# Kernel tuning notes

Measured on AMD Instinct MI355X. Metric: run time of the kernel, lower is better.

The kernel has to match this reference:

```python
import jax, jax.numpy as jnp
import numpy as np

EPS = 1e-5

def _batchnorm1d(x, gamma, beta):
    # x: [B, C, L]; BatchNorm1d(C) training-mode stats over (B, L) per channel
    m = x.mean(axis=(0, 2), keepdims=True)
    v = ((x - m) ** 2).mean(axis=(0, 2), keepdims=True)  # biased variance
    return (x - m) / jnp.sqrt(v + EPS) * gamma[None, :, None] + beta[None, :, None]

def setup_inputs() -> dict:
    key = jax.random.key(0)
    ks = jax.random.split(key, 12)
    B, N, K, D = 1024, 50, 8, 128
    NUM_ENTS, NUM_RELS = 500000, 1000
    inp = {
        'hrt': jax.random.randint(ks[0], (B, 3), 0, NUM_RELS, dtype=jnp.int64) if jax.config.read('jax_enable_x64') else jax.random.randint(ks[0], (B, 3), 0, NUM_RELS).astype(jnp.int32),
        'neb': jax.random.randint(ks[1], (B, N), 0, NUM_ENTS).astype(jnp.int32),
        'nebr': jax.random.randint(ks[2], (B, N, K), 0, NUM_RELS).astype(jnp.int32),
        'adj': jax.random.uniform(ks[3], (B, N + 1, N + 1), dtype=jnp.float32),
        'ent_W': jax.random.normal(ks[4], (NUM_ENTS, D), dtype=jnp.float32) * 0.02,
        'rel_W': jax.random.normal(ks[5], (NUM_RELS, D), dtype=jnp.float32) * 0.02,
        'att_W': jax.random.normal(ks[6], (D, D), dtype=jnp.float32) * (1.0 / np.sqrt(D)),
        'att_b': jnp.zeros((D,), dtype=jnp.float32),
        'gcn_W': jax.random.normal(ks[7], (D, D), dtype=jnp.float32) * (1.0 / np.sqrt(D)),
        'gcn_b': jnp.zeros((D,), dtype=jnp.float32),
        'bn_gamma': jnp.ones((N + 1,), dtype=jnp.float32),
        'bn_beta': jnp.zeros((N + 1,), dtype=jnp.float32),
    }
    return inp

def reference(hrt, neb, nebr, adj, ent_W, rel_W, att_W, att_b, gcn_W, gcn_b, bn_gamma, bn_beta):
    h_em = ent_W[hrt[:, 0]][:, None, :]   # [B,1,D]
    t_em = ent_W[hrt[:, 2]][:, None, :]
    r_em = rel_W[hrt[:, 1]][:, None, :]
    neb_e = ent_W[neb]                    # [B,N,D]
    neb_r_mean = rel_W[nebr].mean(axis=2) # [B,N,D]  (mean over K neighbor relations)
    sum_hrt = (h_em + t_em + r_em) / 3.0  # mean over the 3 stacked rows -> [B,1,D]
    subg = (neb_e + neb_r_mean) / 2.0     # [B,N,D]
    # attention: att_fc applied to query and keys, then bmm
    q = sum_hrt @ att_W.T + att_b         # [B,1,D]
    kmat = subg @ att_W.T + att_b         # [B,N,D]
    att = jnp.einsum('bod,bnd->bn', q, kmat)  # [B,N]
    att = jax.nn.leaky_relu(att, 0.01)
    att = jax.nn.softmax(att, axis=-1)
    subg_w = att[:, :, None] * subg       # [B,N,D]
    x = jnp.concatenate([sum_hrt, subg_w], axis=1)  # [B,N+1,D]
    x = x @ gcn_W.T + gcn_b
    # GCN layer 1 (dropout is identity in eval)
    g1 = _batchnorm1d(jax.nn.relu(jnp.einsum('bij,bjd->bid', adj, x)), bn_gamma, bn_beta)
    # GCN layer 2
    g2 = _batchnorm1d(jax.nn.relu(jnp.einsum('bij,bjd->bid', adj, g1)), bn_gamma, bn_beta)
    tri_em = g2[:, 0:1, :]                # [B,1,D]
    return (h_em, t_em, r_em, tri_em)
```

## Files before the change

### kernel.cpp

```cpp
#include <hip/hip_runtime.h>

#define Bb 1024
#define NN 50
#define KK 8
#define DD 128
#define CC 51

typedef __attribute__((ext_vector_type(8))) short short8;
typedef __attribute__((ext_vector_type(4))) float f32x4;

__device__ __forceinline__ unsigned short f2bf(float f) {
  union { float f; unsigned int u; } un; un.f = f;
  unsigned int r = un.u + 0x7fffu + ((un.u >> 16) & 1u);
  return (unsigned short)(r >> 16);
}
__device__ __forceinline__ float bf2f(unsigned short h) {
  union { unsigned int u; float f; } un; un.u = ((unsigned int)h) << 16;
  return un.f;
}

static constexpr size_t SZ_BCD   = (size_t)Bb * CC * DD;
static constexpr size_t BYTES_H1 = SZ_BCD * 2;
static constexpr size_t OFF_BN   = BYTES_H1;
static constexpr size_t OFF_H2   = OFF_BN + 1024;

__global__ __launch_bounds__(256, 4) void kA_fused(
    const int* __restrict__ hrt, const int* __restrict__ neb,
    const int* __restrict__ nebr, const float* __restrict__ entW,
    const float* __restrict__ relW, const float* __restrict__ attW,
    const float* __restrict__ attb, const float* __restrict__ gcnW,
    const float* __restrict__ gcnb, const float* __restrict__ adj,
    unsigned short* __restrict__ H1bf, float* __restrict__ bn1,
    float* __restrict__ out) {
  int b = blockIdx.x, t = threadIdx.x;
  __shared__ __align__(16) float sub[52 * 132];
  __shared__ float Al[51 * 52];
  __shared__ float sq[DD], sw[DD];
  __shared__ float sl[NN];
  __shared__ float cval;
  unsigned short* Xbl = (unsigned short*)sub;

  for (int idx = t; idx < 51 * 52; idx += 256) {
    int i = idx / 52, j = idx - i * 52;
    Al[idx] = (j < 51) ? adj[(size_t)b * (CC * CC) + i * CC + j] : 0.f;
  }
  if (t < 32) {
    int hi = hrt[b * 3 + 0], ri = hrt[b * 3 + 1], ti = hrt[b * 3 + 2];
    float4 hv = ((const float4*)(entW + (size_t)hi * DD))[t];
    float4 tv = ((const float4*)(entW + (size_t)ti * DD))[t];
    float4 rv = ((const float4*)(relW + (size_t)ri * DD))[t];
    ((float4*)(out + (size_t)b * DD))[t] = hv;
    ((float4*)(out + (size_t)Bb * DD + (size_t)b * DD))[t] = tv;
    ((float4*)(out + (size_t)2 * Bb * DD + (size_t)b * DD))[t] = rv;
    const float inv3 = 1.f / 3.f;
    float4 s;
    s.x = (hv.x + tv.x + rv.x) * inv3;
    s.y = (hv.y + tv.y + rv.y) * inv3;
    s.z = (hv.z + tv.z + rv.z) * inv3;
    s.w = (hv.w + tv.w + rv.w) * inv3;
    ((float4*)sub)[t] = s;
    ((float4*)(sub + 51 * 132))[t] = make_float4(0.f, 0.f, 0.f, 0.f);
  }
  for (int idx = t; idx < NN * 32; idx += 256) {
    int r = idx >> 5, c4 = idx & 31;
    int e = neb[b * NN + r];
    float4 ev = ((const float4*)(entW + (size_t)e * DD))[c4];
    const int* rb = nebr + ((size_t)(b * NN + r)) * KK;
    float4 rs = make_float4(0.f, 0.f, 0.f, 0.f);
#pragma unroll
    for (int k = 0; k < KK; ++k) {
      float4 rv = ((const float4*)(relW + (size_t)rb[k] * DD))[c4];
      rs.x += rv.x; rs.y += rv.y; rs.z += rv.z; rs.w += rv.w;
    }
    float4 sg;
    sg.x = 0.5f * (ev.x + rs.x * 0.125f);
    sg.y = 0.5f * (ev.y + rs.y * 0.125f);
    sg.z = 0.5f * (ev.z + rs.z * 0.125f);
    sg.w = 0.5f * (ev.w + rs.w * 0.125f);
    ((float4*)(sub + (r + 1) * 132))[c4] = sg;
  }
  __syncthreads();
  {
    int wv = t >> 6, l = t & 63, half = l >> 5, l32 = l & 31;
    float4 sv = ((const float4*)sub)[l32];
#pragma unroll 4
    for (int j = 0; j < 16; ++j) {
      int d = 32 * wv + 2 * j + half;
      float4 wr = ((const float4*)(attW + (size_t)d * DD))[l32];
      float p = wr.x * sv.x + wr.y * sv.y + wr.z * sv.z + wr.w * sv.w;
#pragma unroll
      for (int m = 1; m < 32; m <<= 1) p += __shfl_xor(p, m);
      if (l32 == 0) sq[d] = p + attb[d];
    }
  }
  __syncthreads();
  if (t < 128) {
    float w0 = 0.f, w1 = 0.f, w2 = 0.f, w3 = 0.f;
    const float* wc = attW + t;
#pragma unroll 8
    for (int k = 0; k < 128; k += 4) {
      w0 += sq[k]     * wc[(size_t)k * DD];
      w1 += sq[k + 1] * wc[(size_t)(k + 1) * DD];
      w2 += sq[k + 2] * wc[(size_t)(k + 2) * DD];
      w3 += sq[k + 3] * wc[(size_t)(k + 3) * DD];
    }
    sw[t] = (w0 + w1) + (w2 + w3);
  } else if (t < 192) {
    int l = t - 128;
    float v = sq[l] * attb[l] + sq[l + 64] * attb[l + 64];
#pragma unroll
    for (int m = 1; m < 64; m <<= 1) v += __shfl_xor(v, m);
    if (l == 0) cval = v;
  }
  __syncthreads();
  if (t < NN * 4) {
    int n = t >> 2, q = t & 3;
    const float* sg = sub + (n + 1) * 132 + q * 32;
    const float* wq = sw + q * 32;
    float L = 0.f;
#pragma unroll 8
    for (int e = 0; e < 32; ++e) L += sg[e] * wq[e];
    L += __shfl_xor(L, 1);
    L += __shfl_xor(L, 2);
    if (q == 0) {
      L += cval;
      sl[n] = (L > 0.f) ? L : 0.01f * L;
    }
  }
  __syncthreads();
  if (t < 64) {
    float v = (t < NN) ? sl[t] : -1e30f;
    float mx = v;
#pragma unroll
    for (int m = 1; m < 64; m <<= 1) mx = fmaxf(mx, __shfl_xor(mx, m));
    float e = (t < NN) ? __expf(v - mx) : 0.f;
    float sm = e;
#pragma unroll
    for (int m = 1; m < 64; m <<= 1) sm += __shfl_xor(sm, m);
    if (t < NN) sl[t] = e / sm;
  }
  __syncthreads();
  {
    int wv = t >> 6, lane = t & 63;
    int wm = wv >> 1, wn = wv & 1;
    int m16 = lane & 15, g = lane >> 4, q8 = g * 8;
    f32x4 acc[2][4] = {};
    int rowA[2]; float sc[2];
#pragma unroll
    for (int mt = 0; mt < 2; ++mt) {
      int row = wm * 32 + mt * 16 + m16;
      rowA[mt] = (row <= 51) ? row : 51;
      sc[mt] = (row == 0) ? 1.f : ((row <= 50) ? sl[row - 1] : 0.f);
    }
#pragma unroll
    for (int ks = 0; ks < 4; ++ks) {
      short8 afr[2];
#pragma unroll
      for (int mt = 0; mt < 2; ++mt) {
        const float* ap = sub + rowA[mt] * 132 + ks * 32 + q8;
        float4 v0 = ((const float4*)ap)[0];
        float4 v1 = ((const float4*)ap)[1];
        short8 a;
        a[0] = (short)f2bf(sc[mt] * v0.x); a[1] = (short)f2bf(sc[mt] * v0.y);
        a[2] = (short)f2bf(sc[mt] * v0.z); a[3] = (short)f2bf(sc[mt] * v0.w);
        a[4] = (short)f2bf(sc[mt] * v1.x); a[5] = (short)f2bf(sc[mt] * v1.y);
        a[6] = (short)f2bf(sc[mt] * v1.z); a[7] = (short)f2bf(sc[mt] * v1.w);
        afr[mt] = a;
      }
#pragma unroll
      for (int nt = 0; nt < 4; ++nt) {
        int n = wn * 64 + nt * 16 + m16;
        const float* bp = gcnW + (size_t)n * DD + ks * 32 + q8;
        float4 b0 = ((const float4*)bp)[0];
        float4 b1 = ((const float4*)bp)[1];
        short8 bf;
        bf[0] = (short)f2bf(b0.x); bf[1] = (short)f2bf(b0.y);
        bf[2] = (short)f2bf(b0.z); bf[3] = (short)f2bf(b0.w);
        bf[4] = (short)f2bf(b1.x); bf[5] = (short)f2bf(b1.y);
        bf[6] = (short)f2bf(b1.z); bf[7] = (short)f2bf(b1.w);
        acc[0][nt] = __builtin_amdgcn_mfma_f32_16x16x32_bf16(afr[0], bf, acc[0][nt], 0, 0, 0);
        acc[1][nt] = __builtin_amdgcn_mfma_f32_16x16x32_bf16(afr[1], bf, acc[1][nt], 0, 0, 0);
      }
    }
    __syncthreads();
    int qd = g * 4;
#pragma unroll
    for (int mt = 0; mt < 2; ++mt) {
#pragma unroll
      for (int nt = 0; nt < 4; ++nt) {
        int col = wn * 64 + nt * 16 + m16;
        float bias = gcnb[col];
#pragma unroll
        for (int r = 0; r < 4; ++r) {
          int row = wm * 32 + mt * 16 + qd + r;
          if (row < 52) Xbl[row * 136 + col] = f2bf(acc[mt][nt][r] + bias);
        }
      }
    }
  }
  __syncthreads();
  {
    int tc = t & 15, tr = t >> 4;
    float4 acc0[4], acc1[4];
#pragma unroll
    for (int k = 0; k < 4; ++k) {
      acc0[k] = make_float4(0.f, 0.f, 0.f, 0.f);
      acc1[k] = make_float4(0.f, 0.f, 0.f, 0.f);
    }
    for (int jj4 = 0; jj4 < 13; ++jj4) {
      float4 av[4];
#pragma unroll
      for (int k = 0; k < 4; ++k) {
        int i = tr + 16 * k;
        av[k] = (i < 51) ? ((const float4*)(Al + i * 52))[jj4]
                         : make_float4(0.f, 0.f, 0.f, 0.f);
      }
#pragma unroll
      for (int ee = 0; ee < 4; ++ee) {
        int jj = jj4 * 4 + ee;
        uint4 v = ((const uint4*)(Xbl + jj * 136))[tc];
        float f0 = bf2f((unsigned short)(v.x & 0xffff));
        float f1 = bf2f((unsigned short)(v.x >> 16));
        float f2 = bf2f((unsigned short)(v.y & 0xffff));
        float f3 = bf2f((unsigned short)(v.y >> 16));
        float f4 = bf2f((unsigned short)(v.z & 0xffff));
        float f5 = bf2f((unsigned short)(v.z >> 16));
        float f6 = bf2f((unsigned short)(v.w & 0xffff));
        float f7 = bf2f((unsigned short)(v.w >> 16));
#pragma unroll
        for (int k = 0; k < 4; ++k) {
          float a = (ee == 0) ? av[k].x : (ee == 1) ? av[k].y
                    : (ee == 2) ? av[k].z : av[k].w;
          acc0[k].x += a * f0; acc0[k].y += a * f1;
          acc0[k].z += a * f2; acc0[k].w += a * f3;
          acc1[k].x += a * f4; acc1[k].y += a * f5;
          acc1[k].z += a * f6; acc1[k].w += a * f7;
        }
      }
    }
#pragma unroll
    for (int k = 0; k < 4; ++k) {
      int i = tr + 16 * k;
      if (i < 51) {
        float4 h0, h1v;
        h0.x = fmaxf(acc0[k].x, 0.f); h0.y = fmaxf(acc0[k].y, 0.f);
        h0.z = fmaxf(acc0[k].z, 0.f); h0.w = fmaxf(acc0[k].w, 0.f);
        h1v.x = fmaxf(acc1[k].x, 0.f); h1v.y = fmaxf(acc1[k].y, 0.f);
        h1v.z = fmaxf(acc1[k].z, 0.f); h1v.w = fmaxf(acc1[k].w, 0.f);
        size_t rowoff = ((size_t)b * CC + i) * DD;
        ushort4 p0, p1;
        p0.x = f2bf(h0.x); p0.y = f2bf(h0.y); p0.z = f2bf(h0.z); p0.w = f2bf(h0.w);
        p1.x = f2bf(h1v.x); p1.y = f2bf(h1v.y); p1.z = f2bf(h1v.z); p1.w = f2bf(h1v.w);
        ((ushort4*)(H1bf + rowoff))[2 * tc]     = p0;
        ((ushort4*)(H1bf + rowoff))[2 * tc + 1] = p1;
        float s = h0.x + h0.y + h0.z + h0.w + h1v.x + h1v.y + h1v.z + h1v.w;
        float qq = h0.x * h0.x + h0.y * h0.y + h0.z * h0.z + h0.w * h0.w +
                   h1v.x * h1v.x + h1v.y * h1v.y + h1v.z * h1v.z + h1v.w * h1v.w;
#pragma unroll
        for (int m = 1; m < 16; m <<= 1) {
          s += __shfl_xor(s, m);
          qq += __shfl_xor(qq, m);
        }
        if (tc == 0) {
          atomicAdd(&bn1[i], s);
          atomicAdd(&bn1[64 + i], qq);
        }
      }
    }
  }
}

__global__ __launch_bounds__(128) void k6_row0(
    const unsigned short* __restrict__ H1bf, const float* __restrict__ adj,
    const float* __restrict__ bn1, const float* __restrict__ gamma,
    const float* __restrict__ beta, float* __restrict__ h2,
    float* __restrict__ bn2) {
  __shared__ float cj[52];
  __shared__ float td[64];
  __shared__ float reds[128], redq[128];
  int b = blockIdx.x, t = threadIdx.x;
  const float invBD = 1.f / ((float)Bb * (float)DD);
  if (t < 64) td[t] = 0.f;
  if (t < 51) {
    float s = bn1[t], q = bn1[64 + t];
    float m = s * invBD;
    float v = fmaxf(q * invBD - m * m, 0.f);
    float inv = rsqrtf(v + 1e-5f);
    float al = gamma[t] * inv;
    float de = beta[t] - m * al;
    float a0 = adj[(size_t)b * (CC * CC) + t];
    cj[t] = a0 * al;
    td[t] = a0 * de;
  }
  __syncthreads();
  float tcst = 0.f;
  for (int j = 0; j < 51; ++j) tcst += td[j];
  float acc = tcst;
  const unsigned short* hb = H1bf + (size_t)b * CC * DD + t;
#pragma unroll 4
  for (int j = 0; j < 51; ++j) acc += cj[j] * bf2f(hb[(size_t)j * DD]);
  acc = fmaxf(acc, 0.f);
  h2[(size_t)b * DD + t] = acc;
  reds[t] = acc;
  redq[t] = acc * acc;
  __syncthreads();
  for (int s = 64; s > 0; s >>= 1) {
    if (t < s) { reds[t] += reds[t + s]; redq[t] += redq[t + s]; }
    __syncthreads();
  }
  if (t == 0) {
    atomicAdd(&bn2[0], reds[0]);
    atomicAdd(&bn2[1], redq[0]);
  }
}

__global__ __launch_bounds__(256) void k8_final(
    const float* __restrict__ h2, const float* __restrict__ bn2,
    const float* __restrict__ gamma, const float* __restrict__ beta,
    float* __restrict__ out) {
  int i = blockIdx.x * 256 + threadIdx.x;
  const float invBD = 1.f / ((float)Bb * (float)DD);
  float m = bn2[0] * invBD;
  float v = fmaxf(bn2[1] * invBD - m * m, 0.f);
  float inv = rsqrtf(v + 1e-5f);
  out[(size_t)3 * Bb * DD + i] = (h2[i] - m) * inv * gamma[0] + beta[0];
}

extern "C" void kernel_launch(void* const* d_in, const int* in_sizes, int n_in,
                              void* d_out, int out_size, void* d_ws, size_t ws_size,
                              hipStream_t stream) {
  (void)in_sizes; (void)n_in; (void)out_size; (void)ws_size;
  const int*   hrt   = (const int*)d_in[0];
  const int*   neb   = (const int*)d_in[1];
  const int*   nebr  = (const int*)d_in[2];
  const float* adj   = (const float*)d_in[3];
  const float* entW  = (const float*)d_in[4];
  const float* relW  = (const float*)d_in[5];
  const float* attW  = (const float*)d_in[6];
  const float* attb  = (const float*)d_in[7];
  const float* gcnW  = (const float*)d_in[8];
  const float* gcnb  = (const float*)d_in[9];
  const float* gamma = (const float*)d_in[10];
  const float* beta  = (const float*)d_in[11];
  float* out = (float*)d_out;
  char*  ws  = (char*)d_ws;

  unsigned short* H1bf = (unsigned short*)ws;
  float*          bn1  = (float*)(ws + OFF_BN);
  float*          bn2  = bn1 + 128;
  float*          h2   = (float*)(ws + OFF_H2);

  hipMemsetAsync((void*)bn1, 0, 1024, stream);

  kA_fused<<<Bb, 256, 0, stream>>>(hrt, neb, nebr, entW, relW, attW, attb,
                                   gcnW, gcnb, adj, H1bf, bn1, out);
  k6_row0<<<Bb, 128, 0, stream>>>(H1bf, adj, bn1, gamma, beta, h2, bn2);
  k8_final<<<(Bb * DD) / 256, 256, 0, stream>>>(h2, bn2, gamma, beta, out);
}
```

Before: 481.4 us.

## Fuse all stages into one persistent kernel with grid barriers and LDS-resident H1

Merges the three kernels into a single kernel that uses two software grid barriers, one after each BatchNorm statistics accumulation. The bf16 H1 activations stay in shared memory instead of making a round trip through global memory, and the h2 buffer and final elementwise kernel are removed. The intent is to drop two launches and the H1 and h2 global traffic. The cost is that 1024 blocks must all be co-resident for the spin barriers; with launch bounds of 4 blocks per CU on 256 CUs this just fits, and if it does not the kernel deadlocks. Blocks also idle while they spin at each barrier.

After: 677.8 us. 40.8% more time.

```diff
diff --git a/kernel.cpp b/kernel.cpp
--- a/kernel.cpp
+++ b/kernel.cpp
@@ -19,19 +19,28 @@
   return un.f;
 }
 
-static constexpr size_t SZ_BCD   = (size_t)Bb * CC * DD;
-static constexpr size_t BYTES_H1 = SZ_BCD * 2;
-static constexpr size_t OFF_BN   = BYTES_H1;
-static constexpr size_t OFF_H2   = OFF_BN + 1024;
-
-__global__ __launch_bounds__(256, 4) void kA_fused(
+__device__ __forceinline__ void grid_barrier(unsigned* cnt) {
+  __syncthreads();
+  if (threadIdx.x == 0) {
+    __threadfence();
+    atomicAdd(cnt, 1u);
+    while (__hip_atomic_load(cnt, __ATOMIC_RELAXED, __HIP_MEMORY_SCOPE_AGENT) <
+           (unsigned)gridDim.x) {
+      __builtin_amdgcn_s_sleep(2);
+    }
+  }
+  __syncthreads();
+  __threadfence();
+}
+
+__global__ __launch_bounds__(256, 4) void kAll(
     const int* __restrict__ hrt, const int* __restrict__ neb,
     const int* __restrict__ nebr, const float* __restrict__ entW,
     const float* __restrict__ relW, const float* __restrict__ attW,
     const float* __restrict__ attb, const float* __restrict__ gcnW,
     const float* __restrict__ gcnb, const float* __restrict__ adj,
-    unsigned short* __restrict__ H1bf, float* __restrict__ bn1,
-    float* __restrict__ out) {
+    const float* __restrict__ gamma, const float* __restrict__ beta,
+    float* __restrict__ bnbuf, float* __restrict__ out) {
   int b = blockIdx.x, t = threadIdx.x;
   __shared__ __align__(16) float sub[52 * 132];
   __shared__ float Al[51 * 52];
@@ -39,6 +48,9 @@
   __shared__ float sl[NN];
   __shared__ float cval;
   unsigned short* Xbl = (unsigned short*)sub;
+  unsigned short* H1l = (unsigned short*)sub + 7072;
+  unsigned* cnt1 = (unsigned*)(bnbuf + 160);
+  unsigned* cnt2 = (unsigned*)(bnbuf + 161);
 
   for (int idx = t; idx < 51 * 52; idx += 256) {
     int i = idx / 52, j = idx - i * 52;
@@ -247,12 +259,12 @@
         h0.z = fmaxf(acc0[k].z, 0.f); h0.w = fmaxf(acc0[k].w, 0.f);
         h1v.x = fmaxf(acc1[k].x, 0.f); h1v.y = fmaxf(acc1[k].y, 0.f);
         h1v.z = fmaxf(acc1[k].z, 0.f); h1v.w = fmaxf(acc1[k].w, 0.f);
-        size_t rowoff = ((size_t)b * CC + i) * DD;
         ushort4 p0, p1;
         p0.x = f2bf(h0.x); p0.y = f2bf(h0.y); p0.z = f2bf(h0.z); p0.w = f2bf(h0.w);
         p1.x = f2bf(h1v.x); p1.y = f2bf(h1v.y); p1.z = f2bf(h1v.z); p1.w = f2bf(h1v.w);
-        ((ushort4*)(H1bf + rowoff))[2 * tc]     = p0;
-        ((ushort4*)(H1bf + rowoff))[2 * tc + 1] = p1;
+        ushort4* hrow = (ushort4*)(H1l + i * DD);
+        hrow[2 * tc]     = p0;
+        hrow[2 * tc + 1] = p1;
         float s = h0.x + h0.y + h0.z + h0.w + h1v.x + h1v.y + h1v.z + h1v.w;
         float qq = h0.x * h0.x + h0.y * h0.y + h0.z * h0.z + h0.w * h0.w +
                    h1v.x * h1v.x + h1v.y * h1v.y + h1v.z * h1v.z + h1v.w * h1v.w;
@@ -262,68 +274,66 @@
           qq += __shfl_xor(qq, m);
         }
         if (tc == 0) {
-          atomicAdd(&bn1[i], s);
-          atomicAdd(&bn1[64 + i], qq);
+          atomicAdd(&bnbuf[i], s);
+          atomicAdd(&bnbuf[64 + i], qq);
         }
       }
     }
   }
-}
-
-__global__ __launch_bounds__(128) void k6_row0(
-    const unsigned short* __restrict__ H1bf, const float* __restrict__ adj,
-    const float* __restrict__ bn1, const float* __restrict__ gamma,
-    const float* __restrict__ beta, float* __restrict__ h2,
-    float* __restrict__ bn2) {
-  __shared__ float cj[52];
-  __shared__ float td[64];
-  __shared__ float reds[128], redq[128];
-  int b = blockIdx.x, t = threadIdx.x;
-  const float invBD = 1.f / ((float)Bb * (float)DD);
-  if (t < 64) td[t] = 0.f;
-  if (t < 51) {
-    float s = bn1[t], q = bn1[64 + t];
-    float m = s * invBD;
-    float v = fmaxf(q * invBD - m * m, 0.f);
-    float inv = rsqrtf(v + 1e-5f);
-    float al = gamma[t] * inv;
-    float de = beta[t] - m * al;
-    float a0 = adj[(size_t)b * (CC * CC) + t];
-    cj[t] = a0 * al;
-    td[t] = a0 * de;
-  }
-  __syncthreads();
-  float tcst = 0.f;
-  for (int j = 0; j < 51; ++j) tcst += td[j];
-  float acc = tcst;
-  const unsigned short* hb = H1bf + (size_t)b * CC * DD + t;
+  grid_barrier(cnt1);
+  {
+    float* cj = Al;
+    float* td = Al + 64;
+    const float invBD = 1.f / ((float)Bb * (float)DD);
+    if (t < 64) {
+      float a0 = 0.f, al = 0.f, de = 0.f;
+      if (t < 51) {
+        float s = __hip_atomic_load(&bnbuf[t], __ATOMIC_RELAXED, __HIP_MEMORY_SCOPE_AGENT);
+        float q = __hip_atomic_load(&bnbuf[64 + t], __ATOMIC_RELAXED, __HIP_MEMORY_SCOPE_AGENT);
+        float m = s * invBD;
+        float v = fmaxf(q * invBD - m * m, 0.f);
+        float inv = rsqrtf(v + 1e-5f);
+        al = gamma[t] * inv;
+        de = beta[t] - m * al;
+        a0 = adj[(size_t)b * (CC * CC) + t];
+      }
+      cj[t] = a0 * al;
+      td[t] = a0 * de;
+    }
+    __syncthreads();
+    float accv = 0.f;
+    if (t < 128) {
+      float tsum = 0.f;
+      for (int j = 0; j < 51; ++j) tsum += td[j];
+      float acc = tsum;
 #pragma unroll 4
-  for (int j = 0; j < 51; ++j) acc += cj[j] * bf2f(hb[(size_t)j * DD]);
-  acc = fmaxf(acc, 0.f);
-  h2[(size_t)b * DD + t] = acc;
-  reds[t] = acc;
-  redq[t] = acc * acc;
-  __syncthreads();
-  for (int s = 64; s > 0; s >>= 1) {
-    if (t < s) { reds[t] += reds[t + s]; redq[t] += redq[t + s]; }
+      for (int j = 0; j < 51; ++j) acc += cj[j] * bf2f(H1l[j * DD + t]);
+      acc = fmaxf(acc, 0.f);
+      accv = acc;
+      float s_ = acc, q_ = acc * acc;
+#pragma unroll
+      for (int m = 1; m < 64; m <<= 1) {
+        s_ += __shfl_xor(s_, m);
+        q_ += __shfl_xor(q_, m);
+      }
+      if ((t & 63) == 0) { sq[t >> 6] = s_; sw[t >> 6] = q_; }
+    }
     __syncthreads();
-  }
-  if (t == 0) {
-    atomicAdd(&bn2[0], reds[0]);
-    atomicAdd(&bn2[1], redq[0]);
-  }
-}
-
-__global__ __launch_bounds__(256) void k8_final(
-    const float* __restrict__ h2, const float* __restrict__ bn2,
-    const float* __restrict__ gamma, const float* __restrict__ beta,
-    float* __restrict__ out) {
-  int i = blockIdx.x * 256 + threadIdx.x;
-  const float invBD = 1.f / ((float)Bb * (float)DD);
-  float m = bn2[0] * invBD;
-  float v = fmaxf(bn2[1] * invBD - m * m, 0.f);
-  float inv = rsqrtf(v + 1e-5f);
-  out[(size_t)3 * Bb * DD + i] = (h2[i] - m) * inv * gamma[0] + beta[0];
+    if (t == 0) {
+      atomicAdd(&bnbuf[128], sq[0] + sq[1]);
+      atomicAdd(&bnbuf[129], sw[0] + sw[1]);
+    }
+    grid_barrier(cnt2);
+    if (t < 128) {
+      float s2 = __hip_atomic_load(&bnbuf[128], __ATOMIC_RELAXED, __HIP_MEMORY_SCOPE_AGENT);
+      float q2 = __hip_atomic_load(&bnbuf[129], __ATOMIC_RELAXED, __HIP_MEMORY_SCOPE_AGENT);
+      float m2 = s2 * invBD;
+      float v2 = fmaxf(q2 * invBD - m2 * m2, 0.f);
+      float inv2 = rsqrtf(v2 + 1e-5f);
+      out[(size_t)3 * Bb * DD + (size_t)b * DD + t] =
+          (accv - m2) * inv2 * gamma[0] + beta[0];
+    }
+  }
 }
 
 extern "C" void kernel_launch(void* const* d_in, const int* in_sizes, int n_in,
@@ -343,17 +353,10 @@
   const float* gamma = (const float*)d_in[10];
   const float* beta  = (const float*)d_in[11];
   float* out = (float*)d_out;
-  char*  ws  = (char*)d_ws;
-
-  unsigned short* H1bf = (unsigned short*)ws;
-  float*          bn1  = (float*)(ws + OFF_BN);
-  float*          bn2  = bn1 + 128;
-  float*          h2   = (float*)(ws + OFF_H2);
-
-  hipMemsetAsync((void*)bn1, 0, 1024, stream);
-
-  kA_fused<<<Bb, 256, 0, stream>>>(hrt, neb, nebr, entW, relW, attW, attb,
-                                   gcnW, gcnb, adj, H1bf, bn1, out);
-  k6_row0<<<Bb, 128, 0, stream>>>(H1bf, adj, bn1, gamma, beta, h2, bn2);
-  k8_final<<<(Bb * DD) / 256, 256, 0, stream>>>(h2, bn2, gamma, beta, out);
-}
+  float* bnbuf = (float*)d_ws;
+
+  hipMemsetAsync((void*)bnbuf, 0, 1024, stream);
+
+  kAll<<<Bb, 256, 0, stream>>>(hrt, neb, nebr, entW, relW, attW, attb,
+                               gcnW, gcnb, adj, gamma, beta, bnbuf, out);
+}
```
